# Optimization experiments

Hardware: AMD Instinct MI355X
Metric: run time of the kernel (lower is better)

## Reference

```python
import jax, jax.numpy as jnp
import numpy as np

N = 100000       # nodes
E = 1600000      # edges (avg degree 16)
F_IN = 128       # feats_per_node
F1 = 128         # layer_1_feats
F2 = 128         # layer_2_feats


def setup_inputs() -> dict:
    key = jax.random.key(0)
    k1, k2, k3, k4, k5, k6 = jax.random.split(key, 6)
    node_feats = jax.random.normal(k1, (N, F_IN), dtype=jnp.float32)
    # COO representation of sparse normalized adjacency Ahat
    edge_rows = jax.random.randint(k2, (E,), 0, N)
    edge_cols = jax.random.randint(k3, (E,), 0, N)
    edge_vals = jax.random.uniform(k4, (E,), dtype=jnp.float32)
    # reset_param-style init: uniform in +-1/sqrt(fan_in)
    w0 = jax.random.uniform(k5, (F_IN, F1), dtype=jnp.float32,
                            minval=-1.0, maxval=1.0) / np.sqrt(F_IN)
    w1 = jax.random.uniform(k6, (F1, F2), dtype=jnp.float32,
                            minval=-1.0, maxval=1.0) / np.sqrt(F1)
    return {"node_feats": node_feats, "edge_vals": edge_vals,
            "w0": w0, "w1": w1,
            "edge_rows": edge_rows, "edge_cols": edge_cols}


def _spmm(edge_rows, edge_cols, edge_vals, x):
    # out[i] = sum_{(i,j) in edges} val_ij * x[j]   (Ahat @ x)
    msgs = edge_vals[:, None] * x[edge_cols]          # [E, F] gather
    return jax.ops.segment_sum(msgs, edge_rows, num_segments=N)


def reference(node_feats, edge_vals, w0, w1, edge_rows, edge_cols):
    # layer 0: relu(Ahat @ (X @ W0))
    h = jax.nn.relu(_spmm(edge_rows, edge_cols, edge_vals, node_feats @ w0))
    # layer 1: relu(Ahat @ (H @ W1))
    h = jax.nn.relu(_spmm(edge_rows, edge_cols, edge_vals, h @ w1))
    return h
```

## Files before the change

### kernel.cpp

```cpp
#include <hip/hip_runtime.h>

#define N_NODES 100000
#define N_EDGES 1600000
#define F 128
#define M_PAD 100032
#define GEMM_GRID 1563

#define BUCKET_BITS 9
#define BUCKET_SIZE 512
#define NBUCKETS 196
#define BCAP 9216
#define EPB_A 8192
#define ABLOCKS 196

#define AS1 __attribute__((address_space(1)))
#define AS3 __attribute__((address_space(3)))

typedef __attribute__((ext_vector_type(8))) short short8;
typedef __attribute__((ext_vector_type(4))) float f32x4;

__device__ __forceinline__ float bf_lo(unsigned int u) { return __uint_as_float(u << 16); }
__device__ __forceinline__ float bf_hi(unsigned int u) { return __uint_as_float(u & 0xffff0000u); }
__device__ __forceinline__ unsigned short f2bf(float f) {
    unsigned int u = __float_as_uint(f);
    u += 0x7fffu + ((u >> 16) & 1u);
    return (unsigned short)(u >> 16);
}
__device__ __forceinline__ void gload_lds16(const void* g, void* l) {
    __builtin_amdgcn_global_load_lds((const AS1 unsigned int*)g, (AS3 unsigned int*)l, 16, 0, 0);
}

__global__ __launch_bounds__(256) void prep_kernel(const float* __restrict__ W0,
                                                   const float* __restrict__ W1,
                                                   unsigned short* __restrict__ Wt0,
                                                   unsigned short* __restrict__ Wt1,
                                                   int* __restrict__ bucket_cursor) {
    int t = threadIdx.x;
    if (blockIdx.x == 2) {
        if (t < NBUCKETS) bucket_cursor[t] = 0;
        return;
    }
    int c = t & 127;
    int o0 = (t >> 7) * 8;
    if (blockIdx.x == 0) {
        for (int o = o0; o < o0 + 8; ++o) {
            short8 v;
#pragma unroll
            for (int e = 0; e < 8; ++e) v[e] = (short)f2bf(W0[(o * 8 + e) * 128 + c]);
            *(short8*)((char*)Wt0 + c * 256 + ((o * 16) ^ ((c & 7) << 4))) = v;
        }
    } else {
        for (int o = o0; o < o0 + 8; ++o) {
            short8 v;
#pragma unroll
            for (int e = 0; e < 8; ++e) v[e] = (short)f2bf(W1[(o * 8 + e) * 128 + c]);
            *(short8*)&Wt1[c * 128 + o * 8] = v;
        }
    }
}


__device__ __forceinline__ void binA_body(char* smem, int bid,
                                          const int* __restrict__ rows,
                                          const int* __restrict__ cols,
                                          const float* __restrict__ vals,
                                          int* __restrict__ bucket_cursor,
                                          uint2* __restrict__ stage) {
    int* hist = (int*)smem;
    int* base = hist + NBUCKETS;
    int tid = threadIdx.x;
    int start = bid * EPB_A;
    int cnt = min(EPB_A, N_EDGES - start);
    for (int i = tid; i < NBUCKETS; i += 256) hist[i] = 0;
    __syncthreads();
    for (int i = tid; i < cnt; i += 256) atomicAdd(&hist[rows[start + i] >> BUCKET_BITS], 1);
    __syncthreads();
    for (int i = tid; i < NBUCKETS; i += 256) {
        int h = hist[i];
        base[i] = h ? atomicAdd(&bucket_cursor[i], h) : 0;
        hist[i] = 0;
    }
    __syncthreads();
    for (int i = tid; i < cnt; i += 256) {
        int r = rows[start + i];
        int c = cols[start + i];
        unsigned vb = __float_as_uint(vals[start + i]);
        int b = r >> BUCKET_BITS;
        int p = b * BCAP + base[b] + atomicAdd(&hist[b], 1);
        stage[p] = make_uint2(((unsigned)(r & (BUCKET_SIZE - 1)) << 17) | (unsigned)c, vb);
    }
}

__device__ __forceinline__ void gemm0_body(char* smem, int bid,
                                           const float* __restrict__ X,
                                           const unsigned short* __restrict__ Wt0,
                                           unsigned short* __restrict__ T) {
    unsigned short* wlds = (unsigned short*)smem;
    unsigned short* alds = (unsigned short*)(smem + 32768);
    int tid = threadIdx.x;
    int w = tid >> 6, l = tid & 63;
    int q = l >> 4, c16 = l & 15;
    long r0 = (long)bid * 64;

#pragma unroll
    for (int i = 0; i < 8; ++i) {
        int row = w * 32 + i * 4 + q;
        gload_lds16((const char*)Wt0 + row * 256 + c16 * 16,
                    (char*)wlds + (w * 8192 + i * 1024));
    }
#pragma unroll
    for (int i = 0; i < 4; ++i) {
        int row = i * 16 + (tid >> 4);
        int oct = tid & 15;
        long rg = r0 + row;
        if (rg > N_NODES - 1) rg = N_NODES - 1;
        const float4* xp = (const float4*)(X + rg * 128 + oct * 8);
        float4 a = xp[0], bb = xp[1];
        short8 v;
        v[0] = (short)f2bf(a.x); v[1] = (short)f2bf(a.y);
        v[2] = (short)f2bf(a.z); v[3] = (short)f2bf(a.w);
        v[4] = (short)f2bf(bb.x); v[5] = (short)f2bf(bb.y);
        v[6] = (short)f2bf(bb.z); v[7] = (short)f2bf(bb.w);
        *(short8*)((char*)alds + row * 256 + ((oct * 16) ^ ((row & 7) << 4))) = v;
    }
    __syncthreads();

    f32x4 acc[8] = {};
    int nrow = w * 16 + c16;
    int nswz = (nrow & 7) << 4;
#pragma unroll
    for (int ks = 0; ks < 4; ++ks) {
        int kb = ks * 64 + q * 16;
        short8 bfrag = *(const short8*)((const char*)alds + nrow * 256 + (kb ^ nswz));
#pragma unroll
        for (int fb = 0; fb < 8; ++fb) {
            int frow = fb * 16 + c16;
            short8 afrag = *(const short8*)((const char*)wlds + frow * 256 +
                                            (kb ^ ((frow & 7) << 4)));
            acc[fb] = __builtin_amdgcn_mfma_f32_16x16x32_bf16(afrag, bfrag, acc[fb], 0, 0, 0);
        }
    }

    long node = r0 + w * 16 + c16;
#pragma unroll
    for (int fb = 0; fb < 8; ++fb) {
        uint2 o;
        o.x = (unsigned)f2bf(acc[fb][0]) | ((unsigned)f2bf(acc[fb][1]) << 16);
        o.y = (unsigned)f2bf(acc[fb][2]) | ((unsigned)f2bf(acc[fb][3]) << 16);
        *(uint2*)((char*)T + node * 256 + fb * 32 + q * 8) = o;
    }
}

__global__ __launch_bounds__(256) void k1_kernel(const float* __restrict__ X,
                                                 const unsigned short* __restrict__ Wt0,
                                                 unsigned short* __restrict__ T,
                                                 const int* __restrict__ rows,
                                                 const int* __restrict__ cols,
                                                 const float* __restrict__ vals,
                                                 int* __restrict__ bucket_cursor,
                                                 uint2* __restrict__ stage) {
    __shared__ char smem[49152];
    if (blockIdx.x < ABLOCKS) {
        binA_body(smem, blockIdx.x, rows, cols, vals, bucket_cursor, stage);
    } else {
        gemm0_body(smem, blockIdx.x - ABLOCKS, X, Wt0, T);
    }
}

__global__ __launch_bounds__(1024) void binB_kernel(const uint2* __restrict__ stage,
                                                    const int* __restrict__ bucket_cursor,
                                                    uint2* __restrict__ csr,
                                                    uint2* __restrict__ rowseg) {
    __shared__ int hist[BUCKET_SIZE];
    __shared__ int scanv[BUCKET_SIZE];
    __shared__ int cur[BUCKET_SIZE];
    __shared__ int wsum[8], woff[8];
    int b = blockIdx.x;
    int t = threadIdx.x;
    int s0 = b * BCAP;
    int cnt = bucket_cursor[b];
    if (t < BUCKET_SIZE) hist[t] = 0;
    __syncthreads();
    for (int i = t; i < cnt; i += 1024) atomicAdd(&hist[stage[s0 + i].x >> 17], 1);
    __syncthreads();
    int wid = t >> 6, ln = t & 63;
    if (wid < 8) {
        int v = hist[wid * 64 + ln];
#pragma unroll
        for (int d = 1; d < 64; d <<= 1) {
            int u = __shfl_up(v, d);
            if (ln >= d) v += u;
        }
        if (ln == 63) wsum[wid] = v;
        scanv[wid * 64 + ln] = v;
    }
    __syncthreads();
    if (t == 0) {
        int run = 0;
#pragma unroll
        for (int i = 0; i < 8; ++i) { woff[i] = run; run += wsum[i]; }
    }
    __syncthreads();
    if (t < BUCKET_SIZE) {
        int incl = scanv[t] + woff[t >> 6];
        int st = s0 + incl - hist[t];
        cur[t] = st;
        int row = (b << BUCKET_BITS) + t;
        if (row < N_NODES) rowseg[row] = make_uint2((unsigned)st, (unsigned)(st + hist[t]));
    }
    __syncthreads();
    for (int i = t; i < cnt; i += 1024) {
        uint2 e = stage[s0 + i];
        int p = atomicAdd(&cur[e.x >> 17], 1);
        csr[p] = make_uint2(e.x & 0x1FFFFu, e.y);
    }
}

__global__ __launch_bounds__(256) void fused_spmm_gemm_kernel(
        const uint2* __restrict__ rowseg, const uint2* __restrict__ csr,
        const uint2* __restrict__ T2, const unsigned short* __restrict__ Wt1,
        unsigned short* __restrict__ Tout) {
    __shared__ alignas(16) unsigned short alds[64 * 128];
    int tid = threadIdx.x;
    int w = tid >> 6, l = tid & 63;
    int half = l >> 5, fl = l & 31;
    long r0 = (long)blockIdx.x * 64;

    for (int t = 0; t < 16; ++t) {
        int lrow = w * 16 + t;
        long row = r0 + lrow;
        uint2 se = (row < N_NODES) ? rowseg[row] : make_uint2(0u, 0u);
        int s = (int)se.x, e = (int)se.y;
        float a0 = 0.f, a1 = 0.f, a2 = 0.f, a3 = 0.f;
        for (int base = s; base < e; base += 64) {
            int cnt = min(64, e - base);
            uint2 ed = csr[base + l];
            int col_l = (l < cnt) ? (int)ed.x : 0;
            float val_l = (l < cnt) ? __uint_as_float(ed.y) : 0.f;
            int rounds = (cnt + 7) >> 3;
            for (int r = 0; r < rounds; ++r) {
                int j = r * 8;
                int cc[4]; float vv[4]; uint2 xx[4];
#pragma unroll
                for (int i = 0; i < 4; ++i) {
                    cc[i] = __shfl(col_l, j + 2 * i + half);
                    vv[i] = __shfl(val_l, j + 2 * i + half);
                }
#pragma unroll
                for (int i = 0; i < 4; ++i) xx[i] = T2[cc[i] * 32 + fl];
#pragma unroll
                for (int i = 0; i < 4; ++i) {
                    a0 = fmaf(vv[i], bf_lo(xx[i].x), a0);
                    a1 = fmaf(vv[i], bf_hi(xx[i].x), a1);
                    a2 = fmaf(vv[i], bf_lo(xx[i].y), a2);
                    a3 = fmaf(vv[i], bf_hi(xx[i].y), a3);
                }
            }
        }
        a0 += __shfl_xor(a0, 32);
        a1 += __shfl_xor(a1, 32);
        a2 += __shfl_xor(a2, 32);
        a3 += __shfl_xor(a3, 32);
        if (half == 0) {
            a0 = fmaxf(a0, 0.f); a1 = fmaxf(a1, 0.f);
            a2 = fmaxf(a2, 0.f); a3 = fmaxf(a3, 0.f);
            uint2 o;
            o.x = (unsigned)f2bf(a0) | ((unsigned)f2bf(a1) << 16);
            o.y = (unsigned)f2bf(a2) | ((unsigned)f2bf(a3) << 16);
            *(uint2*)((char*)alds + lrow * 256 + ((fl * 8) ^ ((lrow & 7) << 4))) = o;
        }
    }
    __syncthreads();

    int q = l >> 4, c16 = l & 15;
    f32x4 acc[8] = {};
    int nrow = w * 16 + c16;
    int nswz = (nrow & 7) << 4;
#pragma unroll
    for (int ks = 0; ks < 4; ++ks) {
        int kb = ks * 64 + q * 16;
        short8 bfrag = *(const short8*)((const char*)alds + nrow * 256 + (kb ^ nswz));
#pragma unroll
        for (int fb = 0; fb < 8; ++fb) {
            int frow = fb * 16 + c16;
            short8 afrag = *(const short8*)((const char*)Wt1 + frow * 256 + kb);
            acc[fb] = __builtin_amdgcn_mfma_f32_16x16x32_bf16(afrag, bfrag, acc[fb], 0, 0, 0);
        }
    }

    long node = r0 + w * 16 + c16;
#pragma unroll
    for (int fb = 0; fb < 8; ++fb) {
        uint2 o;
        o.x = (unsigned)f2bf(acc[fb][0]) | ((unsigned)f2bf(acc[fb][1]) << 16);
        o.y = (unsigned)f2bf(acc[fb][2]) | ((unsigned)f2bf(acc[fb][3]) << 16);
        *(uint2*)((char*)Tout + node * 256 + fb * 32 + q * 8) = o;
    }
}

__global__ __launch_bounds__(256) void spmm_relu_kernel(const uint2* __restrict__ rowseg,
                                                        const uint2* __restrict__ csr,
                                                        const uint2* __restrict__ T2,
                                                        float* __restrict__ outv) {
    int wave = threadIdx.x >> 6;
    int lane = threadIdx.x & 63;
    int half = lane >> 5;
    int fl = lane & 31;
    int row = blockIdx.x * 4 + wave;
    uint2 se = rowseg[row];
    int s = (int)se.x, e = (int)se.y;
    float a0 = 0.f, a1 = 0.f, a2 = 0.f, a3 = 0.f;
    for (int base = s; base < e; base += 64) {
        int cnt = min(64, e - base);
        uint2 ed = csr[base + lane];
        int col_l = (lane < cnt) ? (int)ed.x : 0;
        float val_l = (lane < cnt) ? __uint_as_float(ed.y) : 0.f;
        int rounds = (cnt + 7) >> 3;
        for (int r = 0; r < rounds; ++r) {
            int j = r * 8;
            int cc[4]; float vv[4]; uint2 xx[4];
#pragma unroll
            for (int i = 0; i < 4; ++i) {
                cc[i] = __shfl(col_l, j + 2 * i + half);
                vv[i] = __shfl(val_l, j + 2 * i + half);
            }
#pragma unroll
            for (int i = 0; i < 4; ++i) xx[i] = T2[cc[i] * 32 + fl];
#pragma unroll
            for (int i = 0; i < 4; ++i) {
                a0 = fmaf(vv[i], bf_lo(xx[i].x), a0);
                a1 = fmaf(vv[i], bf_hi(xx[i].x), a1);
                a2 = fmaf(vv[i], bf_lo(xx[i].y), a2);
                a3 = fmaf(vv[i], bf_hi(xx[i].y), a3);
            }
        }
    }
    a0 += __shfl_xor(a0, 32);
    a1 += __shfl_xor(a1, 32);
    a2 += __shfl_xor(a2, 32);
    a3 += __shfl_xor(a3, 32);
    if (half == 0) {
        *(float4*)(outv + (size_t)row * 128 + fl * 4) =
            make_float4(fmaxf(a0, 0.f), fmaxf(a1, 0.f), fmaxf(a2, 0.f), fmaxf(a3, 0.f));
    }
}

extern "C" void kernel_launch(void* const* d_in, const int* in_sizes, int n_in,
                              void* d_out, int out_size, void* d_ws, size_t ws_size,
                              hipStream_t stream) {
    const float* X     = (const float*)d_in[0];
    const float* evals = (const float*)d_in[1];
    const float* W0    = (const float*)d_in[2];
    const float* W1    = (const float*)d_in[3];
    const int* erows   = (const int*)d_in[4];
    const int* ecols   = (const int*)d_in[5];
    float* out = (float*)d_out;

    char* ws = (char*)d_ws;
    size_t off = 0;
    auto carve = [&](size_t bytes) {
        char* p = ws + off;
        off += (bytes + 255) & ~(size_t)255;
        return p;
    };
    unsigned short* T   = (unsigned short*)carve((size_t)M_PAD * F * 2);
    unsigned short* T2  = (unsigned short*)carve((size_t)M_PAD * F * 2);
    unsigned short* Wt0 = (unsigned short*)carve(128 * 128 * 2);
    unsigned short* Wt1 = (unsigned short*)carve(128 * 128 * 2);
    uint2* stage        = (uint2*)carve((size_t)NBUCKETS * BCAP * 8);
    uint2* csr          = (uint2*)carve(((size_t)NBUCKETS * BCAP + 64) * 8);
    uint2* rowseg       = (uint2*)carve((size_t)N_NODES * 8);
    int* bucket_cursor  = (int*)carve((size_t)NBUCKETS * 4);
    (void)ws_size; (void)in_sizes; (void)n_in; (void)out_size;

    prep_kernel<<<3, 256, 0, stream>>>(W0, W1, Wt0, Wt1, bucket_cursor);

    k1_kernel<<<ABLOCKS + GEMM_GRID, 256, 0, stream>>>(X, Wt0, T, erows, ecols, evals,
                                                       bucket_cursor, stage);

    binB_kernel<<<NBUCKETS, 1024, 0, stream>>>(stage, bucket_cursor, csr, rowseg);

    fused_spmm_gemm_kernel<<<GEMM_GRID, 256, 0, stream>>>(rowseg, csr, (const uint2*)T,
                                                          Wt1, T2);

    spmm_relu_kernel<<<N_NODES / 4, 256, 0, stream>>>(rowseg, csr, (const uint2*)T2, out);
}
```

Before: 223.8 us.

## Split fused SpMM+GEMM into half-wave-per-row SpMM and standalone LDS-staged MFMA GEMM

Replaces the fused layer-1 SpMM+GEMM kernel with three pieces. A templated SpMM kernel assigns one half-wave per row, so each wave handles two rows; it writes a swizzled bf16 H buffer. A separate MFMA GEMM kernel stages both W1 and the H tile into LDS. The final SpMM reuses the half-wave mapping. This removes the serial 16-rows-per-wave loop and the global-memory W1 fragment reads of the fused kernel, and raises parallelism in the gather. The cost is an extra launch and a round trip of H through global memory. W1 is now pre-swizzled in prep the same way as W0.

```diff
diff --git a/kernel.cpp b/kernel.cpp
--- a/kernel.cpp
+++ b/kernel.cpp
@@ -40,22 +40,15 @@
         if (t < NBUCKETS) bucket_cursor[t] = 0;
         return;
     }
+    const float* W = (blockIdx.x == 0) ? W0 : W1;
+    unsigned short* Wt = (blockIdx.x == 0) ? Wt0 : Wt1;
     int c = t & 127;
     int o0 = (t >> 7) * 8;
-    if (blockIdx.x == 0) {
-        for (int o = o0; o < o0 + 8; ++o) {
-            short8 v;
-#pragma unroll
-            for (int e = 0; e < 8; ++e) v[e] = (short)f2bf(W0[(o * 8 + e) * 128 + c]);
-            *(short8*)((char*)Wt0 + c * 256 + ((o * 16) ^ ((c & 7) << 4))) = v;
-        }
-    } else {
-        for (int o = o0; o < o0 + 8; ++o) {
-            short8 v;
-#pragma unroll
-            for (int e = 0; e < 8; ++e) v[e] = (short)f2bf(W1[(o * 8 + e) * 128 + c]);
-            *(short8*)&Wt1[c * 128 + o * 8] = v;
-        }
+    for (int o = o0; o < o0 + 8; ++o) {
+        short8 v;
+#pragma unroll
+        for (int e = 0; e < 8; ++e) v[e] = (short)f2bf(W[(o * 8 + e) * 128 + c]);
+        *(short8*)((char*)Wt + c * 256 + ((o * 16) ^ ((c & 7) << 4))) = v;
     }
 }
 
@@ -167,6 +160,56 @@
     }
 }
 
+__global__ __launch_bounds__(256) void mfma_gemm_kernel(const unsigned short* __restrict__ Av,
+                                                        const unsigned short* __restrict__ Wt,
+                                                        unsigned short* __restrict__ T) {
+    __shared__ alignas(16) unsigned short wlds[128 * 128];
+    __shared__ alignas(16) unsigned short alds[64 * 128];
+    int tid = threadIdx.x;
+    int w = tid >> 6, l = tid & 63;
+    int q = l >> 4, c16 = l & 15;
+    long r0 = (long)blockIdx.x * 64;
+
+#pragma unroll
+    for (int i = 0; i < 8; ++i) {
+        int row = w * 32 + i * 4 + q;
+        gload_lds16((const char*)Wt + row * 256 + c16 * 16,
+                    (char*)wlds + (w * 8192 + i * 1024));
+    }
+#pragma unroll
+    for (int i = 0; i < 4; ++i) {
+        int row = w * 16 + i * 4 + q;
+        gload_lds16((const char*)Av + (r0 + row) * 256 + c16 * 16,
+                    (char*)alds + (w * 4096 + i * 1024));
+    }
+    __syncthreads();
+
+    f32x4 acc[8] = {};
+    int nrow = w * 16 + c16;
+    int nswz = (nrow & 7) << 4;
+#pragma unroll
+    for (int ks = 0; ks < 4; ++ks) {
+        int kb = ks * 64 + q * 16;
+        short8 bfrag = *(const short8*)((const char*)alds + nrow * 256 + (kb ^ nswz));
+#pragma unroll
+        for (int fb = 0; fb < 8; ++fb) {
+            int frow = fb * 16 + c16;
+            short8 afrag = *(const short8*)((const char*)wlds + frow * 256 +
+                                            (kb ^ ((frow & 7) << 4)));
+            acc[fb] = __builtin_amdgcn_mfma_f32_16x16x32_bf16(afrag, bfrag, acc[fb], 0, 0, 0);
+        }
+    }
+
+    long node = r0 + w * 16 + c16;
+#pragma unroll
+    for (int fb = 0; fb < 8; ++fb) {
+        uint2 o;
+        o.x = (unsigned)f2bf(acc[fb][0]) | ((unsigned)f2bf(acc[fb][1]) << 16);
+        o.y = (unsigned)f2bf(acc[fb][2]) | ((unsigned)f2bf(acc[fb][3]) << 16);
+        *(uint2*)((char*)T + node * 256 + fb * 32 + q * 8) = o;
+    }
+}
+
 __global__ __launch_bounds__(1024) void binB_kernel(const uint2* __restrict__ stage,
                                                     const int* __restrict__ bucket_cursor,
                                                     uint2* __restrict__ csr,
@@ -216,113 +259,32 @@
     }
 }
 
-__global__ __launch_bounds__(256) void fused_spmm_gemm_kernel(
-        const uint2* __restrict__ rowseg, const uint2* __restrict__ csr,
-        const uint2* __restrict__ T2, const unsigned short* __restrict__ Wt1,
-        unsigned short* __restrict__ Tout) {
-    __shared__ alignas(16) unsigned short alds[64 * 128];
-    int tid = threadIdx.x;
-    int w = tid >> 6, l = tid & 63;
-    int half = l >> 5, fl = l & 31;
-    long r0 = (long)blockIdx.x * 64;
-
-    for (int t = 0; t < 16; ++t) {
-        int lrow = w * 16 + t;
-        long row = r0 + lrow;
-        uint2 se = (row < N_NODES) ? rowseg[row] : make_uint2(0u, 0u);
-        int s = (int)se.x, e = (int)se.y;
-        float a0 = 0.f, a1 = 0.f, a2 = 0.f, a3 = 0.f;
-        for (int base = s; base < e; base += 64) {
-            int cnt = min(64, e - base);
-            uint2 ed = csr[base + l];
-            int col_l = (l < cnt) ? (int)ed.x : 0;
-            float val_l = (l < cnt) ? __uint_as_float(ed.y) : 0.f;
-            int rounds = (cnt + 7) >> 3;
-            for (int r = 0; r < rounds; ++r) {
-                int j = r * 8;
-                int cc[4]; float vv[4]; uint2 xx[4];
-#pragma unroll
-                for (int i = 0; i < 4; ++i) {
-                    cc[i] = __shfl(col_l, j + 2 * i + half);
-                    vv[i] = __shfl(val_l, j + 2 * i + half);
-                }
-#pragma unroll
-                for (int i = 0; i < 4; ++i) xx[i] = T2[cc[i] * 32 + fl];
-#pragma unroll
-                for (int i = 0; i < 4; ++i) {
-                    a0 = fmaf(vv[i], bf_lo(xx[i].x), a0);
-                    a1 = fmaf(vv[i], bf_hi(xx[i].x), a1);
-                    a2 = fmaf(vv[i], bf_lo(xx[i].y), a2);
-                    a3 = fmaf(vv[i], bf_hi(xx[i].y), a3);
-                }
-            }
-        }
-        a0 += __shfl_xor(a0, 32);
-        a1 += __shfl_xor(a1, 32);
-        a2 += __shfl_xor(a2, 32);
-        a3 += __shfl_xor(a3, 32);
-        if (half == 0) {
-            a0 = fmaxf(a0, 0.f); a1 = fmaxf(a1, 0.f);
-            a2 = fmaxf(a2, 0.f); a3 = fmaxf(a3, 0.f);
-            uint2 o;
-            o.x = (unsigned)f2bf(a0) | ((unsigned)f2bf(a1) << 16);
-            o.y = (unsigned)f2bf(a2) | ((unsigned)f2bf(a3) << 16);
-            *(uint2*)((char*)alds + lrow * 256 + ((fl * 8) ^ ((lrow & 7) << 4))) = o;
-        }
-    }
-    __syncthreads();
-
-    int q = l >> 4, c16 = l & 15;
-    f32x4 acc[8] = {};
-    int nrow = w * 16 + c16;
-    int nswz = (nrow & 7) << 4;
-#pragma unroll
-    for (int ks = 0; ks < 4; ++ks) {
-        int kb = ks * 64 + q * 16;
-        short8 bfrag = *(const short8*)((const char*)alds + nrow * 256 + (kb ^ nswz));
-#pragma unroll
-        for (int fb = 0; fb < 8; ++fb) {
-            int frow = fb * 16 + c16;
-            short8 afrag = *(const short8*)((const char*)Wt1 + frow * 256 + kb);
-            acc[fb] = __builtin_amdgcn_mfma_f32_16x16x32_bf16(afrag, bfrag, acc[fb], 0, 0, 0);
-        }
-    }
-
-    long node = r0 + w * 16 + c16;
-#pragma unroll
-    for (int fb = 0; fb < 8; ++fb) {
-        uint2 o;
-        o.x = (unsigned)f2bf(acc[fb][0]) | ((unsigned)f2bf(acc[fb][1]) << 16);
-        o.y = (unsigned)f2bf(acc[fb][2]) | ((unsigned)f2bf(acc[fb][3]) << 16);
-        *(uint2*)((char*)Tout + node * 256 + fb * 32 + q * 8) = o;
-    }
-}
-
+template <bool OUT_BF16>
 __global__ __launch_bounds__(256) void spmm_relu_kernel(const uint2* __restrict__ rowseg,
                                                         const uint2* __restrict__ csr,
                                                         const uint2* __restrict__ T2,
-                                                        float* __restrict__ outv) {
+                                                        void* __restrict__ outv) {
     int wave = threadIdx.x >> 6;
     int lane = threadIdx.x & 63;
     int half = lane >> 5;
     int fl = lane & 31;
-    int row = blockIdx.x * 4 + wave;
+    int row = blockIdx.x * 8 + wave * 2 + half;
     uint2 se = rowseg[row];
     int s = (int)se.x, e = (int)se.y;
     float a0 = 0.f, a1 = 0.f, a2 = 0.f, a3 = 0.f;
-    for (int base = s; base < e; base += 64) {
-        int cnt = min(64, e - base);
-        uint2 ed = csr[base + lane];
-        int col_l = (lane < cnt) ? (int)ed.x : 0;
-        float val_l = (lane < cnt) ? __uint_as_float(ed.y) : 0.f;
-        int rounds = (cnt + 7) >> 3;
+    for (int base = s; base < e; base += 32) {
+        int cnt = min(32, e - base);
+        uint2 ed = csr[base + fl];
+        int col_l = (fl < cnt) ? (int)ed.x : 0;
+        float val_l = (fl < cnt) ? __uint_as_float(ed.y) : 0.f;
+        int rounds = (cnt + 3) >> 2;
         for (int r = 0; r < rounds; ++r) {
-            int j = r * 8;
+            int j = r * 4;
             int cc[4]; float vv[4]; uint2 xx[4];
 #pragma unroll
             for (int i = 0; i < 4; ++i) {
-                cc[i] = __shfl(col_l, j + 2 * i + half);
-                vv[i] = __shfl(val_l, j + 2 * i + half);
+                cc[i] = __shfl(col_l, j + i, 32);
+                vv[i] = __shfl(val_l, j + i, 32);
             }
 #pragma unroll
             for (int i = 0; i < 4; ++i) xx[i] = T2[cc[i] * 32 + fl];
@@ -335,13 +297,16 @@
             }
         }
     }
-    a0 += __shfl_xor(a0, 32);
-    a1 += __shfl_xor(a1, 32);
-    a2 += __shfl_xor(a2, 32);
-    a3 += __shfl_xor(a3, 32);
-    if (half == 0) {
-        *(float4*)(outv + (size_t)row * 128 + fl * 4) =
-            make_float4(fmaxf(a0, 0.f), fmaxf(a1, 0.f), fmaxf(a2, 0.f), fmaxf(a3, 0.f));
+    a0 = fmaxf(a0, 0.f); a1 = fmaxf(a1, 0.f);
+    a2 = fmaxf(a2, 0.f); a3 = fmaxf(a3, 0.f);
+    if constexpr (OUT_BF16) {
+        uint2 o;
+        o.x = (unsigned)f2bf(a0) | ((unsigned)f2bf(a1) << 16);
+        o.y = (unsigned)f2bf(a2) | ((unsigned)f2bf(a3) << 16);
+        *(uint2*)((char*)outv + (size_t)row * 256 + ((fl * 8) ^ ((row & 7) << 4))) = o;
+    } else {
+        *(float4*)((float*)outv + (size_t)row * 128 + fl * 4) =
+            make_float4(a0, a1, a2, a3);
     }
 }
 
@@ -364,7 +329,7 @@
         return p;
     };
     unsigned short* T   = (unsigned short*)carve((size_t)M_PAD * F * 2);
-    unsigned short* T2  = (unsigned short*)carve((size_t)M_PAD * F * 2);
+    unsigned short* H   = (unsigned short*)carve((size_t)M_PAD * F * 2);
     unsigned short* Wt0 = (unsigned short*)carve(128 * 128 * 2);
     unsigned short* Wt1 = (unsigned short*)carve(128 * 128 * 2);
     uint2* stage        = (uint2*)carve((size_t)NBUCKETS * BCAP * 8);
@@ -380,8 +345,11 @@
 
     binB_kernel<<<NBUCKETS, 1024, 0, stream>>>(stage, bucket_cursor, csr, rowseg);
 
-    fused_spmm_gemm_kernel<<<GEMM_GRID, 256, 0, stream>>>(rowseg, csr, (const uint2*)T,
-                                                          Wt1, T2);
-
-    spmm_relu_kernel<<<N_NODES / 4, 256, 0, stream>>>(rowseg, csr, (const uint2*)T2, out);
-}
+    spmm_relu_kernel<true><<<N_NODES / 8, 256, 0, stream>>>(rowseg, csr,
+                                                            (const uint2*)T, H);
+
+    mfma_gemm_kernel<<<GEMM_GRID, 256, 0, stream>>>(H, Wt1, T);
+
+    spmm_relu_kernel<false><<<N_NODES / 8, 256, 0, stream>>>(rowseg, csr,
+                                                             (const uint2*)T, out);
+}
```

Result: faster. 184.1 us (-17.7%).
